# Kernel optimization log

Measured on AMD Instinct MI355X. Metric: run time of the kernel, lower is better.

## Reference

```python
import jax, jax.numpy as jnp
import numpy as np

N_NODES = 50000
N_EDGES = 1_600_000
F_IN = 128
HIDDEN = 128
N_REL = 8
N_GRAPHS = 64


def setup_inputs() -> dict:
    key = jax.random.key(0)
    ks = jax.random.split(key, 16)
    x = jax.random.normal(ks[0], (N_NODES, F_IN), dtype=jnp.float32)
    edge_index = jax.random.randint(ks[1], (2, N_EDGES), 0, N_NODES, dtype=jnp.int32)
    edge_type = jax.random.randint(ks[2], (N_EDGES,), 0, N_REL, dtype=jnp.int32)
    edge_attr = jax.nn.one_hot(edge_type, N_REL, dtype=jnp.float32)  # one-hot relation encoding
    batch = jnp.sort(jax.random.randint(ks[3], (N_NODES,), 0, N_GRAPHS, dtype=jnp.int32))
    s = 1.0 / np.sqrt(F_IN)
    params = {}
    dims = [(F_IN, HIDDEN), (HIDDEN, HIDDEN), (HIDDEN, HIDDEN)]
    for i, (fi, fo) in enumerate(dims, 1):
        params[f"W{i}"] = jax.random.normal(ks[3 + 3 * i], (N_REL, fi, fo), dtype=jnp.float32) * s
        params[f"root{i}"] = jax.random.normal(ks[4 + 3 * i], (fi, fo), dtype=jnp.float32) * s
        params[f"b{i}"] = jnp.zeros((fo,), dtype=jnp.float32)
    lin_w = jax.random.normal(ks[13], (HIDDEN, HIDDEN), dtype=jnp.float32) * (1.0 / np.sqrt(HIDDEN))
    lin_b = jnp.zeros((HIDDEN,), dtype=jnp.float32)
    return {"x": x, "edge_index": edge_index, "edge_attr": edge_attr, "batch": batch,
            **params, "lin_w": lin_w, "lin_b": lin_b}


def _rgcn_conv(x, src, dst, edge_type, W, root, bias):
    # PyG RGCNConv with aggr='mean': per-relation mean of transformed neighbors + root + bias.
    # Mean is linear, so aggregate raw features per (dst, relation) then apply W_r.
    n = x.shape[0]
    seg = dst * N_REL + edge_type                      # combined segment id [E]
    msg = x[src]                                       # [E, F_in] gather
    agg = jax.ops.segment_sum(msg, seg, num_segments=n * N_REL)
    cnt = jax.ops.segment_sum(jnp.ones((src.shape[0],), x.dtype), seg, num_segments=n * N_REL)
    agg = agg / jnp.maximum(cnt, 1.0)[:, None]
    agg = agg.reshape(n, N_REL, -1)                    # [N, R, F_in]
    return jnp.einsum('nri,rio->no', agg, W) + x @ root + bias


def reference(x, edge_index, edge_attr, batch,
              W1, root1, b1, W2, root2, b2, W3, root3, b3, lin_w, lin_b):
    src, dst = edge_index[0], edge_index[1]
    edge_type = jnp.argmax(edge_attr, axis=1)          # np.where(edge_attr == 1)[1]
    h = jax.nn.relu(_rgcn_conv(x, src, dst, edge_type, W1, root1, b1))
    h = jax.nn.relu(_rgcn_conv(h, src, dst, edge_type, W2, root2, b2))
    h = jax.nn.relu(_rgcn_conv(h, src, dst, edge_type, W3, root3, b3))
    # global_mean_pool over graphs
    sums = jax.ops.segment_sum(h, batch, num_segments=N_GRAPHS)
    cnts = jax.ops.segment_sum(jnp.ones((h.shape[0],), h.dtype), batch, num_segments=N_GRAPHS)
    pooled = sums / jnp.maximum(cnts, 1.0)[:, None]    # [G, hidden]
    return pooled @ lin_w + lin_b
```

## Files before the change

### kernel.cpp

```cpp
#include <hip/hip_runtime.h>
#include <hip/hip_fp16.h>

#define N_NODESC 50000
#define N_EDGESC 1600000
#define FEAT 128
#define NREL 8
#define NSEG (N_NODESC * NREL)
#define NGRAPH 64
#define KTOT 1152
#define NKC 36
#define WPACK_ELEMS (NKC * 4 * 128 * 8)
#define NHALF (N_NODESC * FEAT)

typedef float f32x4 __attribute__((ext_vector_type(4)));
typedef short bf16x8 __attribute__((ext_vector_type(8)));

static inline size_t align256(size_t x) { return (x + 255) & ~(size_t)255; }

__device__ __forceinline__ unsigned short f2bf(float f) {
  unsigned int u = __float_as_uint(f);
  unsigned int r = (u + 0x7fffu + ((u >> 16) & 1u)) >> 16;
  return (unsigned short)r;
}
__device__ __forceinline__ float bf2f(unsigned short h) {
  return __uint_as_float(((unsigned int)h) << 16);
}
__device__ __forceinline__ float4 h4tof4(uint2 r) {
  const __half* h = (const __half*)&r;
  return make_float4(__half2float(h[0]), __half2float(h[1]),
                     __half2float(h[2]), __half2float(h[3]));
}

__global__ void k_zero(int* __restrict__ p, int n) {
  int i = blockIdx.x * blockDim.x + threadIdx.x;
  int stride = gridDim.x * blockDim.x;
  for (; i < n; i += stride) p[i] = 0;
}

__global__ void k_cvt16(const float* __restrict__ in, __half* __restrict__ o) {
  int i = blockIdx.x * blockDim.x + threadIdx.x;
  if (i * 4 >= NHALF) return;
  float4 v = *(const float4*)&in[i * 4];
  __half h[4] = {__float2half(v.x), __float2half(v.y), __float2half(v.z), __float2half(v.w)};
  *(uint2*)&o[(size_t)i * 4] = *(uint2*)h;
}

__global__ void k_edge_hist(const int* __restrict__ ei, const float* __restrict__ eattr,
                            int* __restrict__ seg, int* __restrict__ cnt) {
  int e = blockIdx.x * blockDim.x + threadIdx.x;
  if (e >= N_EDGESC) return;
  int dst = ei[N_EDGESC + e];
  const float4* ap = (const float4*)(eattr + (size_t)e * 8);
  float4 a0 = ap[0], a1 = ap[1];
  int ty = 0;
  if (a0.y > 0.5f) ty = 1;
  if (a0.z > 0.5f) ty = 2;
  if (a0.w > 0.5f) ty = 3;
  if (a1.x > 0.5f) ty = 4;
  if (a1.y > 0.5f) ty = 5;
  if (a1.z > 0.5f) ty = 6;
  if (a1.w > 0.5f) ty = 7;
  int s = dst * NREL + ty;
  seg[e] = s;
  atomicAdd(&cnt[s], 1);
}

__global__ void k_scan1(const int* __restrict__ cnt, int* __restrict__ outIncl,
                        int* __restrict__ bsums, int n) {
  __shared__ int sd[256];
  int t = threadIdx.x;
  int base = blockIdx.x * 4096 + t * 16;
  int v[16];
  int s = 0;
#pragma unroll
  for (int j = 0; j < 16; ++j) {
    int idx = base + j;
    int x = (idx < n) ? cnt[idx] : 0;
    s += x;
    v[j] = s;
  }
  sd[t] = s;
  __syncthreads();
  for (int off = 1; off < 256; off <<= 1) {
    int add = (t >= off) ? sd[t - off] : 0;
    __syncthreads();
    sd[t] += add;
    __syncthreads();
  }
  int prev = (t > 0) ? sd[t - 1] : 0;
#pragma unroll
  for (int j = 0; j < 16; ++j) {
    int idx = base + j;
    if (idx < n) outIncl[idx] = prev + v[j];
  }
  if (t == 255) bsums[blockIdx.x] = sd[255];
}

__global__ void k_scan2(int* __restrict__ bsums, int nb) {
  __shared__ int sd[128];
  int t = threadIdx.x;
  int v = (t < nb) ? bsums[t] : 0;
  sd[t] = v;
  __syncthreads();
  for (int off = 1; off < 128; off <<= 1) {
    int add = (t >= off) ? sd[t - off] : 0;
    __syncthreads();
    sd[t] += add;
    __syncthreads();
  }
  if (t < nb) bsums[t] = sd[t] - v;
}

__global__ void k_scan3(int* __restrict__ offsets, const int* __restrict__ bsums, int n) {
  int i = blockIdx.x * blockDim.x + threadIdx.x;
  if (i == 0) offsets[0] = 0;
  if (i < n) offsets[i + 1] += bsums[i >> 12];
}

__global__ void k_scatter(const int* __restrict__ ei, const int* __restrict__ seg,
                          const int* __restrict__ offsets, int* __restrict__ cursor,
                          int* __restrict__ ssrc) {
  int e = blockIdx.x * blockDim.x + threadIdx.x;
  if (e >= N_EDGESC) return;
  int s = seg[e];
  int p = offsets[s] + atomicAdd(&cursor[s], 1);
  ssrc[p] = ei[e];
}

__global__ __launch_bounds__(256, 8) void k_agg(
    const __half* __restrict__ in, const int* __restrict__ offsets,
    const int* __restrict__ ssrc, __half* __restrict__ agg,
    int segBase, int segCount) {
  int t = blockIdx.x * blockDim.x + threadIdx.x;
  int ul = t >> 5;
  int l = t & 31;
  if (ul >= segCount) return;
  int u = segBase + ul;
  int beg = offsets[u], end = offsets[u + 1];
  float4 s = make_float4(0.f, 0.f, 0.f, 0.f);
  for (int base = beg; base < end; base += 4) {
    int last = end - 1;
    int e1 = base + 1 <= last ? base + 1 : last;
    int e2 = base + 2 <= last ? base + 2 : last;
    int e3 = base + 3 <= last ? base + 3 : last;
    int i0 = ssrc[base], i1 = ssrc[e1], i2 = ssrc[e2], i3 = ssrc[e3];
    uint2 r0 = *(const uint2*)&in[(size_t)i0 * FEAT + l * 4];
    uint2 r1 = *(const uint2*)&in[(size_t)i1 * FEAT + l * 4];
    uint2 r2 = *(const uint2*)&in[(size_t)i2 * FEAT + l * 4];
    uint2 r3 = *(const uint2*)&in[(size_t)i3 * FEAT + l * 4];
    float4 v0 = h4tof4(r0), v1 = h4tof4(r1), v2 = h4tof4(r2), v3 = h4tof4(r3);
    s.x += v0.x; s.y += v0.y; s.z += v0.z; s.w += v0.w;
    if (base + 1 < end) { s.x += v1.x; s.y += v1.y; s.z += v1.z; s.w += v1.w; }
    if (base + 2 < end) { s.x += v2.x; s.y += v2.y; s.z += v2.z; s.w += v2.w; }
    if (base + 3 < end) { s.x += v3.x; s.y += v3.y; s.z += v3.z; s.w += v3.w; }
  }
  int c = end - beg;
  if (c > 1) {
    float inv = 1.0f / (float)c;
    s.x *= inv; s.y *= inv; s.z *= inv; s.w *= inv;
  }
  __half hv[4] = {__float2half(s.x), __float2half(s.y), __float2half(s.z), __float2half(s.w)};
  *(uint2*)&agg[(size_t)ul * FEAT + l * 4] = *(uint2*)hv;
}

__global__ void k_wpack(const float* __restrict__ W, const float* __restrict__ root,
                        unsigned short* __restrict__ whi, unsigned short* __restrict__ wlo) {
  int idx = blockIdx.x * 256 + threadIdx.x;
  if (idx >= WPACK_ELEMS) return;
  int j = idx & 7;
  int n = (idx >> 3) & 127;
  int slot = idx >> 10;
  int k = slot * 8 + j;
  float v = (k < 1024) ? W[(size_t)k * 128 + n] : root[(size_t)(k - 1024) * 128 + n];
  unsigned short hi = f2bf(v);
  float lof = v - bf2f(hi);
  whi[idx] = hi;
  wlo[idx] = f2bf(lof);
}

__global__ __launch_bounds__(256, 2) void k_gemm_mfma(
    const __half* __restrict__ aggc,
    const __half* __restrict__ xin,
    const unsigned short* __restrict__ Whi, const unsigned short* __restrict__ Wlo,
    const float* __restrict__ bias, __half* __restrict__ out16,
    int n0g, int rows) {
  __shared__ unsigned short Ahi[4 * 128 * 8] __attribute__((aligned(16)));
  __shared__ unsigned short Alo[4 * 128 * 8] __attribute__((aligned(16)));
  __shared__ unsigned short Bhi[4 * 128 * 8] __attribute__((aligned(16)));
  __shared__ unsigned short Blo[4 * 128 * 8] __attribute__((aligned(16)));

  const int t = threadIdx.x;
  const int lane = t & 63, wave = t >> 6;
  const int l15 = lane & 15, lg = lane >> 4;
  const int wrow0 = wave * 32;
  const int m0 = blockIdx.x * 128;
  const int srow = t >> 1, half = t & 1;

  f32x4 acc[2][8];
#pragma unroll
  for (int a = 0; a < 2; ++a)
#pragma unroll
    for (int b = 0; b < 8; ++b) acc[a][b] = (f32x4){0.f, 0.f, 0.f, 0.f};

  for (int kc = 0; kc < NKC; ++kc) {
    int rowc = srow;
    if (m0 + rowc >= rows) rowc = rows - 1 - m0;
    if (rowc < 0) rowc = 0;
    const __half* asrc = (kc < 32)
        ? (aggc + (size_t)(m0 + rowc) * 1024 + kc * 32 + half * 16)
        : (xin + (size_t)(n0g + m0 + rowc) * FEAT + (kc - 32) * 32 + half * 16);
    uint4 av0 = ((const uint4*)asrc)[0];
    uint4 av1 = ((const uint4*)asrc)[1];
    const uint4* bhs = (const uint4*)(Whi + (size_t)kc * 4096);
    const uint4* bls = (const uint4*)(Wlo + (size_t)kc * 4096);
    uint4 bh0 = bhs[t * 2], bh1 = bhs[t * 2 + 1];
    uint4 bl0 = bls[t * 2], bl1 = bls[t * 2 + 1];

    __syncthreads();

    __half avbuf[16];
    *(uint4*)&avbuf[0] = av0;
    *(uint4*)&avbuf[8] = av1;
#pragma unroll
    for (int gg = 0; gg < 2; ++gg) {
      union { unsigned short u[8]; uint4 v; } ph, pl;
#pragma unroll
      for (int j = 0; j < 8; ++j) {
        float f = __half2float(avbuf[gg * 8 + j]);
        unsigned short hi = f2bf(f);
        ph.u[j] = hi;
        pl.u[j] = f2bf(f - bf2f(hi));
      }
      int g = half * 2 + gg;
      *(uint4*)&Ahi[((size_t)(g * 128 + srow)) * 8] = ph.v;
      *(uint4*)&Alo[((size_t)(g * 128 + srow)) * 8] = pl.v;
    }
    ((uint4*)Bhi)[t * 2] = bh0;
    ((uint4*)Bhi)[t * 2 + 1] = bh1;
    ((uint4*)Blo)[t * 2] = bl0;
    ((uint4*)Blo)[t * 2 + 1] = bl1;

    __syncthreads();

    bf16x8 ah[2], al[2];
#pragma unroll
    for (int mf = 0; mf < 2; ++mf) {
      int ar = wrow0 + mf * 16 + l15;
      ah[mf] = *(const bf16x8*)&Ahi[((size_t)(lg * 128 + ar)) * 8];
      al[mf] = *(const bf16x8*)&Alo[((size_t)(lg * 128 + ar)) * 8];
    }
#pragma unroll
    for (int nf = 0; nf < 8; ++nf) {
      int bn = nf * 16 + l15;
      bf16x8 bh = *(const bf16x8*)&Bhi[((size_t)(lg * 128 + bn)) * 8];
      bf16x8 bl = *(const bf16x8*)&Blo[((size_t)(lg * 128 + bn)) * 8];
#pragma unroll
      for (int mf = 0; mf < 2; ++mf) {
        acc[mf][nf] = __builtin_amdgcn_mfma_f32_16x16x32_bf16(ah[mf], bh, acc[mf][nf], 0, 0, 0);
        acc[mf][nf] = __builtin_amdgcn_mfma_f32_16x16x32_bf16(ah[mf], bl, acc[mf][nf], 0, 0, 0);
        acc[mf][nf] = __builtin_amdgcn_mfma_f32_16x16x32_bf16(al[mf], bh, acc[mf][nf], 0, 0, 0);
      }
    }
  }

  float bcol[8];
#pragma unroll
  for (int nf = 0; nf < 8; ++nf) bcol[nf] = bias[nf * 16 + l15];
#pragma unroll
  for (int mf = 0; mf < 2; ++mf)
#pragma unroll
    for (int nf = 0; nf < 8; ++nf)
#pragma unroll
      for (int j = 0; j < 4; ++j) {
        int grow = m0 + wrow0 + mf * 16 + lg * 4 + j;
        if (grow < rows) {
          float v = acc[mf][nf][j] + bcol[nf];
          v = v > 0.f ? v : 0.f;
          out16[(size_t)(n0g + grow) * FEAT + nf * 16 + l15] = __float2half(v);
        }
      }
}

__global__ void k_pool(const __half* __restrict__ h, const int* __restrict__ batch,
                       const float* __restrict__ lw, const float* __restrict__ lb,
                       float* __restrict__ out) {
  __shared__ float sums[8][128];
  __shared__ float prow[128];
  int gidx = blockIdx.x, t = threadIdx.x;
  int f = t & 127, grp = t >> 7;
  int lo = 0, hi = N_NODESC;
  while (lo < hi) {
    int mid = (lo + hi) >> 1;
    if (batch[mid] < gidx) lo = mid + 1; else hi = mid;
  }
  int start = lo;
  hi = N_NODESC;
  while (lo < hi) {
    int mid = (lo + hi) >> 1;
    if (batch[mid] < gidx + 1) lo = mid + 1; else hi = mid;
  }
  int end = lo;
  float s = 0.f;
  for (int n = start + grp; n < end; n += 8) s += __half2float(h[(size_t)n * FEAT + f]);
  sums[grp][f] = s;
  __syncthreads();
  if (grp == 0) {
    float tot = 0.f;
#pragma unroll
    for (int gg = 0; gg < 8; ++gg) tot += sums[gg][f];
    int c = end - start;
    prow[f] = (c > 0) ? tot / (float)c : 0.f;
  }
  __syncthreads();
  float a = 0.f;
  for (int k = grp * 16; k < grp * 16 + 16; ++k) a = fmaf(prow[k], lw[(size_t)k * FEAT + f], a);
  __syncthreads();
  sums[grp][f] = a;
  __syncthreads();
  if (grp == 0) {
    float tot = lb[f];
#pragma unroll
    for (int gg = 0; gg < 8; ++gg) tot += sums[gg][f];
    out[(size_t)gidx * FEAT + f] = tot;
  }
}

extern "C" void kernel_launch(void* const* d_in, const int* in_sizes, int n_in,
                              void* d_out, int out_size, void* d_ws, size_t ws_size,
                              hipStream_t stream) {
  const float* x = (const float*)d_in[0];
  const int* ei = (const int*)d_in[1];
  const float* eattr = (const float*)d_in[2];
  const int* batch = (const int*)d_in[3];
  const float* Wl[3] = {(const float*)d_in[4], (const float*)d_in[7], (const float*)d_in[10]};
  const float* rl[3] = {(const float*)d_in[5], (const float*)d_in[8], (const float*)d_in[11]};
  const float* bl[3] = {(const float*)d_in[6], (const float*)d_in[9], (const float*)d_in[12]};
  const float* lw = (const float*)d_in[13];
  const float* lb = (const float*)d_in[14];
  float* out = (float*)d_out;
  (void)n_in; (void)in_sizes; (void)out_size;

  size_t pos = 0;
  char* base = (char*)d_ws;
  auto alloc = [&](size_t bytes) { char* q = base + pos; pos += align256(bytes); return q; };
  int* seg = (int*)alloc(sizeof(int) * (size_t)N_EDGESC);
  int* cntcur = (int*)alloc(sizeof(int) * (size_t)2 * NSEG);
  int* cnt = cntcur;
  int* cursor = cntcur + NSEG;
  int* offsets = (int*)alloc(sizeof(int) * (size_t)(NSEG + 1));
  int* bsums = (int*)alloc(sizeof(int) * 1024);
  int* ssrc = (int*)alloc(sizeof(int) * (size_t)N_EDGESC);
  __half* p0 = (__half*)alloc(sizeof(__half) * (size_t)NHALF);
  __half* p1 = (__half*)alloc(sizeof(__half) * (size_t)NHALF);
  unsigned short* whi = (unsigned short*)alloc(sizeof(unsigned short) * (size_t)WPACK_ELEMS);
  unsigned short* wlo = (unsigned short*)alloc(sizeof(unsigned short) * (size_t)WPACK_ELEMS);
  size_t remain = (ws_size > pos) ? (ws_size - pos) : 0;
  long long cn = (long long)(remain / (sizeof(__half) * NREL * FEAT));
  int chunkNodes = (cn > N_NODESC) ? N_NODESC : (int)cn;
  chunkNodes &= ~127;
  if (chunkNodes < 128) chunkNodes = 128;
  __half* aggbuf = (__half*)(base + pos);
  int nchunks = (N_NODESC + chunkNodes - 1) / chunkNodes;

  hipLaunchKernelGGL(k_zero, dim3(2048), dim3(256), 0, stream, cntcur, 2 * NSEG);
  hipLaunchKernelGGL(k_edge_hist, dim3((N_EDGESC + 255) / 256), dim3(256), 0, stream,
                     ei, eattr, seg, cnt);
  int nbScan = (NSEG + 4095) / 4096;
  hipLaunchKernelGGL(k_scan1, dim3(nbScan), dim3(256), 0, stream, cnt, offsets + 1, bsums, NSEG);
  hipLaunchKernelGGL(k_scan2, dim3(1), dim3(128), 0, stream, bsums, nbScan);
  hipLaunchKernelGGL(k_scan3, dim3((NSEG + 255) / 256), dim3(256), 0, stream, offsets, bsums, NSEG);
  hipLaunchKernelGGL(k_scatter, dim3((N_EDGESC + 255) / 256), dim3(256), 0, stream,
                     ei, seg, offsets, cursor, ssrc);

  hipLaunchKernelGGL(k_cvt16, dim3((NHALF / 4 + 255) / 256), dim3(256), 0, stream, x, p0);

  const __half* inPtr = p0;
  __half* outPtr = p1;
  for (int L = 0; L < 3; ++L) {
    hipLaunchKernelGGL(k_wpack, dim3((WPACK_ELEMS + 255) / 256), dim3(256), 0, stream,
                       Wl[L], rl[L], whi, wlo);
    for (int c = 0; c < nchunks; ++c) {
      int nodeBase = c * chunkNodes;
      int rowsC = N_NODESC - nodeBase;
      if (rowsC > chunkNodes) rowsC = chunkNodes;
      int segCount = rowsC * NREL;
      int aggBlocks = (segCount * 32 + 255) / 256;
      hipLaunchKernelGGL(k_agg, dim3(aggBlocks), dim3(256), 0, stream,
                         inPtr, offsets, ssrc, aggbuf, nodeBase * NREL, segCount);
      hipLaunchKernelGGL(k_gemm_mfma, dim3((rowsC + 127) / 128), dim3(256), 0, stream,
                         aggbuf, inPtr, whi, wlo, bl[L], outPtr, nodeBase, rowsC);
    }
    const __half* tmp = inPtr;
    inPtr = outPtr;
    outPtr = (__half*)tmp;
  }

  hipLaunchKernelGGL(k_pool, dim3(NGRAPH), dim3(1024), 0, stream, p1, batch, lw, lb, out);
}
```

Before: 852.9 us.

## Use fp16 MFMA with split weights and per-node aggregation loop

Switches the GEMM from three bf16 MFMAs with hi/lo splits of both operands to two fp16 MFMAs, since the activations are already fp16 and need no split. This removes the per-element A conversion and the Alo shared buffer, and launch bounds are raised to 4 blocks per SM. The aggregation kernel now assigns one 32-lane group per node and loops over the 8 relations, instead of one group per (node, relation) segment. That cuts the thread count by 8x and serialises the relation loop, which may reduce the parallelism available to hide gather latency.

```diff
diff --git a/kernel.cpp b/kernel.cpp
--- a/kernel.cpp
+++ b/kernel.cpp
@@ -13,18 +13,10 @@
 #define NHALF (N_NODESC * FEAT)
 
 typedef float f32x4 __attribute__((ext_vector_type(4)));
-typedef short bf16x8 __attribute__((ext_vector_type(8)));
+typedef _Float16 f16x8 __attribute__((ext_vector_type(8)));
 
 static inline size_t align256(size_t x) { return (x + 255) & ~(size_t)255; }
 
-__device__ __forceinline__ unsigned short f2bf(float f) {
-  unsigned int u = __float_as_uint(f);
-  unsigned int r = (u + 0x7fffu + ((u >> 16) & 1u)) >> 16;
-  return (unsigned short)r;
-}
-__device__ __forceinline__ float bf2f(unsigned short h) {
-  return __uint_as_float(((unsigned int)h) << 16);
-}
 __device__ __forceinline__ float4 h4tof4(uint2 r) {
   const __half* h = (const __half*)&r;
   return make_float4(__half2float(h[0]), __half2float(h[1]),
@@ -130,41 +122,44 @@
 __global__ __launch_bounds__(256, 8) void k_agg(
     const __half* __restrict__ in, const int* __restrict__ offsets,
     const int* __restrict__ ssrc, __half* __restrict__ agg,
-    int segBase, int segCount) {
+    int nodeBase, int nodeCount) {
   int t = blockIdx.x * blockDim.x + threadIdx.x;
-  int ul = t >> 5;
+  int un = t >> 5;
   int l = t & 31;
-  if (ul >= segCount) return;
-  int u = segBase + ul;
-  int beg = offsets[u], end = offsets[u + 1];
-  float4 s = make_float4(0.f, 0.f, 0.f, 0.f);
-  for (int base = beg; base < end; base += 4) {
-    int last = end - 1;
-    int e1 = base + 1 <= last ? base + 1 : last;
-    int e2 = base + 2 <= last ? base + 2 : last;
-    int e3 = base + 3 <= last ? base + 3 : last;
-    int i0 = ssrc[base], i1 = ssrc[e1], i2 = ssrc[e2], i3 = ssrc[e3];
-    uint2 r0 = *(const uint2*)&in[(size_t)i0 * FEAT + l * 4];
-    uint2 r1 = *(const uint2*)&in[(size_t)i1 * FEAT + l * 4];
-    uint2 r2 = *(const uint2*)&in[(size_t)i2 * FEAT + l * 4];
-    uint2 r3 = *(const uint2*)&in[(size_t)i3 * FEAT + l * 4];
-    float4 v0 = h4tof4(r0), v1 = h4tof4(r1), v2 = h4tof4(r2), v3 = h4tof4(r3);
-    s.x += v0.x; s.y += v0.y; s.z += v0.z; s.w += v0.w;
-    if (base + 1 < end) { s.x += v1.x; s.y += v1.y; s.z += v1.z; s.w += v1.w; }
-    if (base + 2 < end) { s.x += v2.x; s.y += v2.y; s.z += v2.z; s.w += v2.w; }
-    if (base + 3 < end) { s.x += v3.x; s.y += v3.y; s.z += v3.z; s.w += v3.w; }
-  }
-  int c = end - beg;
-  if (c > 1) {
-    float inv = 1.0f / (float)c;
-    s.x *= inv; s.y *= inv; s.z *= inv; s.w *= inv;
-  }
-  __half hv[4] = {__float2half(s.x), __float2half(s.y), __float2half(s.z), __float2half(s.w)};
-  *(uint2*)&agg[(size_t)ul * FEAT + l * 4] = *(uint2*)hv;
+  if (un >= nodeCount) return;
+  int node = nodeBase + un;
+  for (int r = 0; r < NREL; ++r) {
+    int sidx = node * NREL + r;
+    int beg = offsets[sidx], end = offsets[sidx + 1];
+    float4 s = make_float4(0.f, 0.f, 0.f, 0.f);
+    for (int base = beg; base < end; base += 4) {
+      int last = end - 1;
+      int e1 = base + 1 <= last ? base + 1 : last;
+      int e2 = base + 2 <= last ? base + 2 : last;
+      int e3 = base + 3 <= last ? base + 3 : last;
+      int i0 = ssrc[base], i1 = ssrc[e1], i2 = ssrc[e2], i3 = ssrc[e3];
+      uint2 r0 = *(const uint2*)&in[(size_t)i0 * FEAT + l * 4];
+      uint2 r1 = *(const uint2*)&in[(size_t)i1 * FEAT + l * 4];
+      uint2 r2 = *(const uint2*)&in[(size_t)i2 * FEAT + l * 4];
+      uint2 r3 = *(const uint2*)&in[(size_t)i3 * FEAT + l * 4];
+      float4 v0 = h4tof4(r0), v1 = h4tof4(r1), v2 = h4tof4(r2), v3 = h4tof4(r3);
+      s.x += v0.x; s.y += v0.y; s.z += v0.z; s.w += v0.w;
+      if (base + 1 < end) { s.x += v1.x; s.y += v1.y; s.z += v1.z; s.w += v1.w; }
+      if (base + 2 < end) { s.x += v2.x; s.y += v2.y; s.z += v2.z; s.w += v2.w; }
+      if (base + 3 < end) { s.x += v3.x; s.y += v3.y; s.z += v3.z; s.w += v3.w; }
+    }
+    int c = end - beg;
+    if (c > 1) {
+      float inv = 1.0f / (float)c;
+      s.x *= inv; s.y *= inv; s.z *= inv; s.w *= inv;
+    }
+    __half hv[4] = {__float2half(s.x), __float2half(s.y), __float2half(s.z), __float2half(s.w)};
+    *(uint2*)&agg[((size_t)un * NREL + r) * FEAT + l * 4] = *(uint2*)hv;
+  }
 }
 
 __global__ void k_wpack(const float* __restrict__ W, const float* __restrict__ root,
-                        unsigned short* __restrict__ whi, unsigned short* __restrict__ wlo) {
+                        __half* __restrict__ whi, __half* __restrict__ wlo) {
   int idx = blockIdx.x * 256 + threadIdx.x;
   if (idx >= WPACK_ELEMS) return;
   int j = idx & 7;
@@ -172,22 +167,21 @@
   int slot = idx >> 10;
   int k = slot * 8 + j;
   float v = (k < 1024) ? W[(size_t)k * 128 + n] : root[(size_t)(k - 1024) * 128 + n];
-  unsigned short hi = f2bf(v);
-  float lof = v - bf2f(hi);
+  __half hi = __float2half(v);
+  float lof = v - __half2float(hi);
   whi[idx] = hi;
-  wlo[idx] = f2bf(lof);
-}
-
-__global__ __launch_bounds__(256, 2) void k_gemm_mfma(
+  wlo[idx] = __float2half(lof);
+}
+
+__global__ __launch_bounds__(256, 4) void k_gemm_mfma(
     const __half* __restrict__ aggc,
     const __half* __restrict__ xin,
-    const unsigned short* __restrict__ Whi, const unsigned short* __restrict__ Wlo,
+    const __half* __restrict__ Whi, const __half* __restrict__ Wlo,
     const float* __restrict__ bias, __half* __restrict__ out16,
     int n0g, int rows) {
-  __shared__ unsigned short Ahi[4 * 128 * 8] __attribute__((aligned(16)));
-  __shared__ unsigned short Alo[4 * 128 * 8] __attribute__((aligned(16)));
-  __shared__ unsigned short Bhi[4 * 128 * 8] __attribute__((aligned(16)));
-  __shared__ unsigned short Blo[4 * 128 * 8] __attribute__((aligned(16)));
+  __shared__ __half Ah[4 * 128 * 8] __attribute__((aligned(16)));
+  __shared__ __half Bh[4 * 128 * 8] __attribute__((aligned(16)));
+  __shared__ __half Bl[4 * 128 * 8] __attribute__((aligned(16)));
 
   const int t = threadIdx.x;
   const int lane = t & 63, wave = t >> 6;
@@ -218,47 +212,32 @@
 
     __syncthreads();
 
-    __half avbuf[16];
-    *(uint4*)&avbuf[0] = av0;
-    *(uint4*)&avbuf[8] = av1;
-#pragma unroll
-    for (int gg = 0; gg < 2; ++gg) {
-      union { unsigned short u[8]; uint4 v; } ph, pl;
-#pragma unroll
-      for (int j = 0; j < 8; ++j) {
-        float f = __half2float(avbuf[gg * 8 + j]);
-        unsigned short hi = f2bf(f);
-        ph.u[j] = hi;
-        pl.u[j] = f2bf(f - bf2f(hi));
-      }
-      int g = half * 2 + gg;
-      *(uint4*)&Ahi[((size_t)(g * 128 + srow)) * 8] = ph.v;
-      *(uint4*)&Alo[((size_t)(g * 128 + srow)) * 8] = pl.v;
-    }
-    ((uint4*)Bhi)[t * 2] = bh0;
-    ((uint4*)Bhi)[t * 2 + 1] = bh1;
-    ((uint4*)Blo)[t * 2] = bl0;
-    ((uint4*)Blo)[t * 2 + 1] = bl1;
-
-    __syncthreads();
-
-    bf16x8 ah[2], al[2];
+    {
+      int g0 = half * 2;
+      *(uint4*)&Ah[((size_t)(g0 * 128 + srow)) * 8] = av0;
+      *(uint4*)&Ah[((size_t)((g0 + 1) * 128 + srow)) * 8] = av1;
+      ((uint4*)Bh)[t * 2] = bh0;
+      ((uint4*)Bh)[t * 2 + 1] = bh1;
+      ((uint4*)Bl)[t * 2] = bl0;
+      ((uint4*)Bl)[t * 2 + 1] = bl1;
+    }
+    __syncthreads();
+
+    f16x8 af[2];
 #pragma unroll
     for (int mf = 0; mf < 2; ++mf) {
       int ar = wrow0 + mf * 16 + l15;
-      ah[mf] = *(const bf16x8*)&Ahi[((size_t)(lg * 128 + ar)) * 8];
-      al[mf] = *(const bf16x8*)&Alo[((size_t)(lg * 128 + ar)) * 8];
+      af[mf] = *(const f16x8*)&Ah[((size_t)(lg * 128 + ar)) * 8];
     }
 #pragma unroll
     for (int nf = 0; nf < 8; ++nf) {
       int bn = nf * 16 + l15;
-      bf16x8 bh = *(const bf16x8*)&Bhi[((size_t)(lg * 128 + bn)) * 8];
-      bf16x8 bl = *(const bf16x8*)&Blo[((size_t)(lg * 128 + bn)) * 8];
+      f16x8 bh = *(const f16x8*)&Bh[((size_t)(lg * 128 + bn)) * 8];
+      f16x8 bl = *(const f16x8*)&Bl[((size_t)(lg * 128 + bn)) * 8];
 #pragma unroll
       for (int mf = 0; mf < 2; ++mf) {
-        acc[mf][nf] = __builtin_amdgcn_mfma_f32_16x16x32_bf16(ah[mf], bh, acc[mf][nf], 0, 0, 0);
-        acc[mf][nf] = __builtin_amdgcn_mfma_f32_16x16x32_bf16(ah[mf], bl, acc[mf][nf], 0, 0, 0);
-        acc[mf][nf] = __builtin_amdgcn_mfma_f32_16x16x32_bf16(al[mf], bh, acc[mf][nf], 0, 0, 0);
+        acc[mf][nf] = __builtin_amdgcn_mfma_f32_16x16x32_f16(af[mf], bh, acc[mf][nf], 0, 0, 0);
+        acc[mf][nf] = __builtin_amdgcn_mfma_f32_16x16x32_f16(af[mf], bl, acc[mf][nf], 0, 0, 0);
       }
     }
   }
@@ -352,8 +331,8 @@
   int* ssrc = (int*)alloc(sizeof(int) * (size_t)N_EDGESC);
   __half* p0 = (__half*)alloc(sizeof(__half) * (size_t)NHALF);
   __half* p1 = (__half*)alloc(sizeof(__half) * (size_t)NHALF);
-  unsigned short* whi = (unsigned short*)alloc(sizeof(unsigned short) * (size_t)WPACK_ELEMS);
-  unsigned short* wlo = (unsigned short*)alloc(sizeof(unsigned short) * (size_t)WPACK_ELEMS);
+  __half* whi = (__half*)alloc(sizeof(__half) * (size_t)WPACK_ELEMS);
+  __half* wlo = (__half*)alloc(sizeof(__half) * (size_t)WPACK_ELEMS);
   size_t remain = (ws_size > pos) ? (ws_size - pos) : 0;
   long long cn = (long long)(remain / (sizeof(__half) * NREL * FEAT));
   int chunkNodes = (cn > N_NODESC) ? N_NODESC : (int)cn;
@@ -383,10 +362,9 @@
       int nodeBase = c * chunkNodes;
       int rowsC = N_NODESC - nodeBase;
       if (rowsC > chunkNodes) rowsC = chunkNodes;
-      int segCount = rowsC * NREL;
-      int aggBlocks = (segCount * 32 + 255) / 256;
+      int aggBlocks = (rowsC * 32 + 255) / 256;
       hipLaunchKernelGGL(k_agg, dim3(aggBlocks), dim3(256), 0, stream,
-                         inPtr, offsets, ssrc, aggbuf, nodeBase * NREL, segCount);
+                         inPtr, offsets, ssrc, aggbuf, nodeBase, rowsC);
       hipLaunchKernelGGL(k_gemm_mfma, dim3((rowsC + 127) / 128), dim3(256), 0, stream,
                          aggbuf, inPtr, whi, wlo, bl[L], outPtr, nodeBase, rowsC);
     }
```

Measured after the change: 790.0 us. 7.4% less time.
